# Optimization experiments

Hardware: AMD Instinct MI355X
Metric: run time of the kernel (lower is better)

The kernel has to match this reference:

```python
import jax, jax.numpy as jnp
import numpy as np

B, FEAT, FIELD, K = 16384, 2048, 32, 64

def setup_inputs() -> dict:
    key = jax.random.key(0)
    k1, k2, k3, k4 = jax.random.split(key, 4)
    x = jax.random.normal(k1, (B, FEAT), dtype=jnp.float32)
    # nn.Linear(feature_size, 1): weight [1, FEAT] (use vector), bias [1] (scalar)
    w = jax.random.normal(k2, (FEAT,), dtype=jnp.float32) / np.sqrt(FEAT)
    b = jax.random.normal(k3, (), dtype=jnp.float32)
    # v ~ N(0, 0.01) as in torch.normal(0, 0.01, ...)
    v = 0.01 * jax.random.normal(k4, (FEAT, FIELD, K), dtype=jnp.float32)
    return {"x": x, "w": w, "b": b, "v": v}

def reference(x, w, b, v):
    # linear part: Linear(feature_size, 1).squeeze() -> [B]
    linear_part = x @ w + b  # [B]
    # field_x = tensordot(x, v, dims=1) -> [B, FIELD, K]
    field_x = jnp.einsum('bf,fsk->bsk', x, v)
    # sum_{i<j} sum_k f_i * f_j  ==  0.5 * (||sum_i f_i||^2 - sum_i ||f_i||^2)
    s = field_x.sum(axis=1)                      # [B, K]
    sq = (field_x * field_x).sum(axis=(1, 2))    # [B]
    interaction = 0.5 * ((s * s).sum(axis=-1) - sq)  # [B]
    return jax.nn.sigmoid(linear_part + interaction)
```

## Files before the change

### kernel.cpp

```cpp
#include <hip/hip_runtime.h>
#include <cstdint>
#include <cstddef>

#define B_ROWS 16384
#define FEAT   2048
#define FIELD  32
#define KDIM   64
#define NCOLS  2048
#define NAUG   2176

using half8   = __attribute__((ext_vector_type(8))) _Float16;
using half4   = __attribute__((ext_vector_type(4))) _Float16;
using floatx4 = __attribute__((ext_vector_type(4))) float;

__device__ __forceinline__ void load_lds16(const void* g, void* l) {
  __builtin_amdgcn_global_load_lds((const __attribute__((address_space(1))) void*)g,
                                   (__attribute__((address_space(3))) void*)l, 16, 0, 0);
}

__global__ __launch_bounds__(256) void k_prep_v(const float* __restrict__ v,
                                                const float* __restrict__ w,
                                                _Float16* __restrict__ vt,
                                                float* __restrict__ arg) {
  const int bb = blockIdx.x;
  const int t = threadIdx.x;
  if (bb < 1024) {
    __shared__ _Float16 tile[64 * 68];
    const int f0 = (bb >> 5) * 64;
    const int n0 = (bb & 31) * 64;
#pragma unroll
    for (int j = 0; j < 4; ++j) {
      int c = j * 256 + t;
      int row = c >> 4;
      int col = (c & 15) * 4;
      float4 val = *(const float4*)(v + (size_t)(f0 + row) * NCOLS + n0 + col);
      tile[row * 68 + col + 0] = (_Float16)val.x;
      tile[row * 68 + col + 1] = (_Float16)val.y;
      tile[row * 68 + col + 2] = (_Float16)val.z;
      tile[row * 68 + col + 3] = (_Float16)val.w;
    }
    __syncthreads();
#pragma unroll
    for (int j = 0; j < 4; ++j) {
      int c = j * 256 + t;
      int nl = c >> 4;
      int fl = (c & 15) * 4;
      half4 h = { tile[(fl + 0) * 68 + nl], tile[(fl + 1) * 68 + nl],
                  tile[(fl + 2) * 68 + nl], tile[(fl + 3) * 68 + nl] };
      *(half4*)(vt + (size_t)(n0 + nl) * FEAT + f0 + fl) = h;
    }
  } else if (bb < 1536) {
    const int k = t & 63;
    const int f = (bb - 1024) * 4 + (t >> 6);
    float s = 0.f;
#pragma unroll
    for (int si = 0; si < FIELD; ++si) s += v[(size_t)f * NCOLS + si * KDIM + k];
    vt[(size_t)(NCOLS + k) * FEAT + f] = (_Float16)s;
  } else if (bb < 2048) {
    int idx = (bb - 1536) * 256 + t;
    int r = NCOLS + KDIM + (idx >> 11);
    int f = idx & 2047;
    vt[(size_t)r * FEAT + f] = (r == NCOLS + KDIM) ? (_Float16)w[f] : (_Float16)0.f;
  } else {
    arg[(bb - 2048) * 256 + t] = 0.f;
  }
}

__global__ __launch_bounds__(256) void k_prep_xa(const float* __restrict__ x,
                                                 const _Float16* __restrict__ vt,
                                                 _Float16* __restrict__ xh,
                                                 float* __restrict__ arg) {
  __shared__ __align__(16) _Float16 lds_a[32 * 64];
  __shared__ __align__(16) _Float16 lds_b[128 * 64];
  const int t = threadIdx.x;
  const int m0 = blockIdx.x * 32;
  const int lane = t & 63;
  const int wave = t >> 6;
  const int wm = (wave & 1) * 16;
  const int wn = (wave >> 1) * 64;
  const int lr = lane & 15;
  const int lk = (lane >> 4) * 8;

  const int arow = t >> 3;
  const int akc  = t & 7;
  const float*    xsrc = x  + (size_t)(m0 + arow) * FEAT + akc * 8;
  _Float16*       xdst = xh + (size_t)(m0 + arow) * FEAT + akc * 8;
  _Float16*       adst = lds_a + arow * 64 + (akc ^ (arow & 7)) * 8;

  floatx4 acc[4] = {};

  for (int k0 = 0; k0 < FEAT; k0 += 64) {
    float4 va = *(const float4*)(xsrc + k0);
    float4 vb = *(const float4*)(xsrc + k0 + 4);
    half8 h = { (_Float16)va.x, (_Float16)va.y, (_Float16)va.z, (_Float16)va.w,
                (_Float16)vb.x, (_Float16)vb.y, (_Float16)vb.z, (_Float16)vb.w };
    *(half8*)(xdst + k0) = h;
    *(half8*)adst = h;
#pragma unroll
    for (int i = 0; i < 4; ++i) {
      int c = i * 256 + t;
      int row = c >> 3;
      int g = (c & 7) ^ (row & 7);
      load_lds16(vt + (size_t)(NCOLS + row) * FEAT + k0 + g * 8, lds_b + c * 8);
    }
    __syncthreads();
#pragma unroll
    for (int ks = 0; ks < 64; ks += 32) {
      const int kc = (ks + lk) >> 3;
      const int ma = wm + lr;
      half8 af = *(const half8*)(lds_a + ma * 64 + (kc ^ (ma & 7)) * 8);
      half8 bf[4];
#pragma unroll
      for (int f = 0; f < 4; ++f) {
        int nb = wn + f * 16 + lr;
        bf[f] = *(const half8*)(lds_b + nb * 64 + (kc ^ (nb & 7)) * 8);
      }
#pragma unroll
      for (int fn = 0; fn < 4; ++fn)
        acc[fn] = __builtin_amdgcn_mfma_f32_16x16x32_f16(af, bf[fn],
                                                         acc[fn], 0, 0, 0);
    }
    __syncthreads();
  }

  const int cq = lane >> 4;
#pragma unroll
  for (int r = 0; r < 4; ++r) {
    float contrib = 0.f;
#pragma unroll
    for (int fn = 0; fn < 4; ++fn) {
      int col = wn + fn * 16 + lr;
      float vv = acc[fn][r];
      if (col < KDIM)            contrib += 0.5f * vv * vv;
      else if (col == KDIM)      contrib += vv;
    }
    contrib += __shfl_xor(contrib, 1);
    contrib += __shfl_xor(contrib, 2);
    contrib += __shfl_xor(contrib, 4);
    contrib += __shfl_xor(contrib, 8);
    if (lr == 0) atomicAdd(&arg[m0 + wm + cq * 4 + r], contrib);
  }
}

__global__ __launch_bounds__(512, 2) void k_gemm(const _Float16* __restrict__ xh,
                                                 const _Float16* __restrict__ vt,
                                                 float* __restrict__ arg) {
  __shared__ __align__(16) _Float16 lds[65536];
  const int tid  = threadIdx.x;
  const int lane = tid & 63;
  const int wave = tid >> 6;
  const int wm   = wave >> 2;
  const int wn   = wave & 3;
  const int lr   = lane & 15;
  const int q    = lane >> 4;

  const int bid = blockIdx.x;
  const int wg  = (bid & 7) * 64 + (bid >> 3);
  const int ng  = wg >> 7;
  const int rem = wg & 127;
  const int mi  = rem >> 1;
  const int nr  = rem & 1;
  const int m0  = mi * 256;
  const int n0  = (ng * 2 + nr) * 256;

  int offA[4], offB[4];
#pragma unroll
  for (int f = 0; f < 4; ++f) {
    int L = f * 16 + lr;
    int u = wm * 4 + q;
    offA[f] = L * 64 + ((u ^ (L & 7)) * 8);
  }
#pragma unroll
  for (int g = 0; g < 4; ++g) {
    int L = (wn & 1) * 64 + g * 16 + lr;
    int u = (wn >> 1) * 4 + q;
    offB[g] = L * 64 + ((u ^ (L & 7)) * 8);
  }

  const int L0   = tid >> 3;
  const int u0   = (tid & 7) ^ (L0 & 7);
  const int row0 = (u0 >> 2) * 128 + L0;
  const int kc0  = u0 & 3;
  const _Float16* pA0 = xh + (size_t)(m0 + row0) * FEAT + kc0 * 8;
  const _Float16* pA1 = pA0 + (size_t)64 * FEAT;
  const _Float16* pB0 = vt + (size_t)(n0 + row0) * FEAT + kc0 * 8;
  const _Float16* pB1 = pB0 + (size_t)64 * FEAT;

  auto stageA = [&](int koff, int seg) {
    load_lds16(pA0 + koff, lds + seg + tid * 8);
    load_lds16(pA1 + koff, lds + seg + 4096 + tid * 8);
  };
  auto stageB = [&](int koff, int seg) {
    load_lds16(pB0 + koff, lds + seg + tid * 8);
    load_lds16(pB1 + koff, lds + seg + 4096 + tid * 8);
  };

  floatx4 acc[8][4] = {};
  half8 af[4], bf[4];

  stageA(0, 0);       stageB(0, 32768);
  stageA(32, 8192);   stageB(32, 40960);
  stageA(64, 16384);  stageB(64, 49152);
  asm volatile("s_waitcnt vmcnt(4)" ::: "memory");
  __builtin_amdgcn_s_barrier();

#define PHASE_TAIL()                                        \
    __builtin_amdgcn_s_barrier();                           \
    asm volatile("s_waitcnt lgkmcnt(0)" ::: "memory");      \
    __builtin_amdgcn_sched_barrier(0);                      \
    __builtin_amdgcn_s_setprio(1)

#define PHASE_END()                                         \
    __builtin_amdgcn_s_setprio(0);                          \
    __builtin_amdgcn_s_barrier()

#pragma unroll 2
  for (int t = 0; t < 32; ++t) {
    const int sA0  = ((t & 1) << 1) * 8192;
    const int sB0  = 32768 + sA0;
    const int sPA1 = ((((t + 1) & 1) << 1) | 1) * 8192;

#pragma unroll
    for (int g = 0; g < 4; ++g) bf[g] = *(const half8*)(lds + sB0 + offB[g]);
#pragma unroll
    for (int f = 0; f < 4; ++f) af[f] = *(const half8*)(lds + sA0 + offA[f]);
    if (t < 31) stageA((t + 1) * 64 + 32, sPA1);
    PHASE_TAIL();
#pragma unroll
    for (int f = 0; f < 4; ++f)
#pragma unroll
      for (int g = 0; g < 4; ++g)
        acc[f][g] = __builtin_amdgcn_mfma_f32_16x16x32_f16(af[f], bf[g],
                                                           acc[f][g], 0, 0, 0);
    PHASE_END();

#pragma unroll
    for (int f = 0; f < 4; ++f) af[f] = *(const half8*)(lds + sA0 + 4096 + offA[f]);
    if (t < 31) stageB((t + 1) * 64 + 32, 32768 + sPA1);
    PHASE_TAIL();
#pragma unroll
    for (int f = 0; f < 4; ++f)
#pragma unroll
      for (int g = 0; g < 4; ++g)
        acc[4 + f][g] = __builtin_amdgcn_mfma_f32_16x16x32_f16(af[f], bf[g],
                                                               acc[4 + f][g], 0, 0, 0);
    PHASE_END();

#pragma unroll
    for (int g = 0; g < 4; ++g) bf[g] = *(const half8*)(lds + sB0 + 8192 + offB[g]);
#pragma unroll
    for (int f = 0; f < 4; ++f) af[f] = *(const half8*)(lds + sA0 + 8192 + offA[f]);
    if (t < 30) stageA((t + 2) * 64, sA0);
    PHASE_TAIL();
#pragma unroll
    for (int f = 0; f < 4; ++f)
#pragma unroll
      for (int g = 0; g < 4; ++g)
        acc[f][g] = __builtin_amdgcn_mfma_f32_16x16x32_f16(af[f], bf[g],
                                                           acc[f][g], 0, 0, 0);
    PHASE_END();

#pragma unroll
    for (int f = 0; f < 4; ++f) af[f] = *(const half8*)(lds + sA0 + 12288 + offA[f]);
    if (t < 30) stageB((t + 2) * 64, sB0);
    __builtin_amdgcn_s_barrier();
    asm volatile("s_waitcnt lgkmcnt(0)" ::: "memory");
    __builtin_amdgcn_sched_barrier(0);
    __builtin_amdgcn_s_setprio(1);
#pragma unroll
    for (int f = 0; f < 4; ++f)
#pragma unroll
      for (int g = 0; g < 4; ++g)
        acc[4 + f][g] = __builtin_amdgcn_mfma_f32_16x16x32_f16(af[f], bf[g],
                                                               acc[4 + f][g], 0, 0, 0);
    __builtin_amdgcn_s_setprio(0);
    if (t < 30) { asm volatile("s_waitcnt vmcnt(4)" ::: "memory"); }
    else        { asm volatile("s_waitcnt vmcnt(0)" ::: "memory"); }
    __builtin_amdgcn_sched_barrier(0);
    __builtin_amdgcn_s_barrier();
  }
#undef PHASE_TAIL
#undef PHASE_END

  const int cq = lane >> 4;
  const int mrow = m0 + wm * 128;
#pragma unroll
  for (int f = 0; f < 8; ++f) {
#pragma unroll
    for (int r = 0; r < 4; ++r) {
      float contrib = 0.f;
#pragma unroll
      for (int g = 0; g < 4; ++g) {
        float vv = acc[f][g][r];
        contrib -= 0.5f * vv * vv;
      }
      contrib += __shfl_xor(contrib, 1);
      contrib += __shfl_xor(contrib, 2);
      contrib += __shfl_xor(contrib, 4);
      contrib += __shfl_xor(contrib, 8);
      if (lr == 0) atomicAdd(&arg[mrow + f * 16 + cq * 4 + r], contrib);
    }
  }
}

__global__ __launch_bounds__(256) void k_fin(const float* __restrict__ arg,
                                             const float* __restrict__ b,
                                             float* __restrict__ out) {
  int i = blockIdx.x * 256 + threadIdx.x;
  float z = arg[i] + b[0];
  out[i] = 1.f / (1.f + __expf(-z));
}

extern "C" void kernel_launch(void* const* d_in, const int* in_sizes, int n_in,
                              void* d_out, int out_size, void* d_ws, size_t ws_size,
                              hipStream_t stream) {
  const float* x = (const float*)d_in[0];
  const float* w = (const float*)d_in[1];
  const float* b = (const float*)d_in[2];
  const float* v = (const float*)d_in[3];
  float* out = (float*)d_out;

  char* ws = (char*)d_ws;
  _Float16* xh  = (_Float16*)ws;
  _Float16* vt  = (_Float16*)(ws + 67108864);
  float*    arg = (float*)(ws + 67108864 + 8912896);

  k_prep_v<<<2112, 256, 0, stream>>>(v, w, vt, arg);
  k_prep_xa<<<512, 256, 0, stream>>>(x, vt, xh, arg);
  k_gemm<<<512, 512, 0, stream>>>(xh, vt, arg);
  k_fin<<<64, 256, 0, stream>>>(arg, b, out);
}
```

Measured before the change: 354.9 us.

## Double-buffer MFMA fragments so LDS reads overlap the previous MFMA phase

```diff
diff --git a/kernel.cpp b/kernel.cpp
--- a/kernel.cpp
+++ b/kernel.cpp
@@ -142,6 +142,14 @@
   }
 }
 
+#define NT 32
+
+#define VMCNT(N) asm volatile("s_waitcnt vmcnt(" #N ")" ::: "memory")
+#define LGKM0()  asm volatile("s_waitcnt lgkmcnt(0)" ::: "memory")
+#define SCHED0() __builtin_amdgcn_sched_barrier(0)
+#define BARRIER() __builtin_amdgcn_s_barrier()
+#define PRIO(N) __builtin_amdgcn_s_setprio(N)
+
 __global__ __launch_bounds__(512, 2) void k_gemm(const _Float16* __restrict__ xh,
                                                  const _Float16* __restrict__ vt,
                                                  float* __restrict__ arg) {
@@ -196,91 +204,93 @@
   };
 
   floatx4 acc[8][4] = {};
-  half8 af[4], bf[4];
+  half8 afP[4], afQ[4], bf0[4], bf1[4];
 
   stageA(0, 0);       stageB(0, 32768);
   stageA(32, 8192);   stageB(32, 40960);
   stageA(64, 16384);  stageB(64, 49152);
-  asm volatile("s_waitcnt vmcnt(4)" ::: "memory");
-  __builtin_amdgcn_s_barrier();
-
-#define PHASE_TAIL()                                        \
-    __builtin_amdgcn_s_barrier();                           \
-    asm volatile("s_waitcnt lgkmcnt(0)" ::: "memory");      \
-    __builtin_amdgcn_sched_barrier(0);                      \
-    __builtin_amdgcn_s_setprio(1)
-
-#define PHASE_END()                                         \
-    __builtin_amdgcn_s_setprio(0);                          \
-    __builtin_amdgcn_s_barrier()
+  VMCNT(8);
+  BARRIER();
+  SCHED0();
+#pragma unroll
+  for (int f = 0; f < 4; ++f) afP[f] = *(const half8*)(lds + offA[f]);
+#pragma unroll
+  for (int g = 0; g < 4; ++g) bf0[g] = *(const half8*)(lds + 32768 + offB[g]);
 
 #pragma unroll 2
-  for (int t = 0; t < 32; ++t) {
-    const int sA0  = ((t & 1) << 1) * 8192;
+  for (int t = 0; t < NT; ++t) {
+    const int sA0  = (t & 1) << 14;
+    const int sA1  = sA0 + 8192;
     const int sB0  = 32768 + sA0;
-    const int sPA1 = ((((t + 1) & 1) << 1) | 1) * 8192;
-
-#pragma unroll
-    for (int g = 0; g < 4; ++g) bf[g] = *(const half8*)(lds + sB0 + offB[g]);
-#pragma unroll
-    for (int f = 0; f < 4; ++f) af[f] = *(const half8*)(lds + sA0 + offA[f]);
-    if (t < 31) stageA((t + 1) * 64 + 32, sPA1);
-    PHASE_TAIL();
+    const int sB1  = sB0 + 8192;
+    const int nsA0 = sA0 ^ 16384;
+    const int nsA1 = nsA0 + 8192;
+    const int nsB0 = 32768 + nsA0;
+    const int nsB1 = nsB0 + 8192;
+
+    BARRIER(); SCHED0();
+#pragma unroll
+    for (int f = 0; f < 4; ++f) afQ[f] = *(const half8*)(lds + sA0 + 4096 + offA[f]);
+    if (t + 1 < NT) stageA((t + 1) * 64 + 32, nsA1);
+    SCHED0(); PRIO(1);
 #pragma unroll
     for (int f = 0; f < 4; ++f)
 #pragma unroll
       for (int g = 0; g < 4; ++g)
-        acc[f][g] = __builtin_amdgcn_mfma_f32_16x16x32_f16(af[f], bf[g],
+        acc[f][g] = __builtin_amdgcn_mfma_f32_16x16x32_f16(afP[f], bf0[g],
                                                            acc[f][g], 0, 0, 0);
-    PHASE_END();
-
-#pragma unroll
-    for (int f = 0; f < 4; ++f) af[f] = *(const half8*)(lds + sA0 + 4096 + offA[f]);
-    if (t < 31) stageB((t + 1) * 64 + 32, 32768 + sPA1);
-    PHASE_TAIL();
+    PRIO(0); SCHED0();
+    LGKM0();
+    if (t < NT - 1) { VMCNT(6); } else { VMCNT(0); }
+
+    BARRIER(); SCHED0();
+#pragma unroll
+    for (int f = 0; f < 4; ++f) afP[f] = *(const half8*)(lds + sA1 + offA[f]);
+#pragma unroll
+    for (int g = 0; g < 4; ++g) bf1[g] = *(const half8*)(lds + sB1 + offB[g]);
+    if (t + 1 < NT) stageB((t + 1) * 64 + 32, nsB1);
+    SCHED0(); PRIO(1);
 #pragma unroll
     for (int f = 0; f < 4; ++f)
 #pragma unroll
       for (int g = 0; g < 4; ++g)
-        acc[4 + f][g] = __builtin_amdgcn_mfma_f32_16x16x32_f16(af[f], bf[g],
+        acc[4 + f][g] = __builtin_amdgcn_mfma_f32_16x16x32_f16(afQ[f], bf0[g],
                                                                acc[4 + f][g], 0, 0, 0);
-    PHASE_END();
-
-#pragma unroll
-    for (int g = 0; g < 4; ++g) bf[g] = *(const half8*)(lds + sB0 + 8192 + offB[g]);
-#pragma unroll
-    for (int f = 0; f < 4; ++f) af[f] = *(const half8*)(lds + sA0 + 8192 + offA[f]);
-    if (t < 30) stageA((t + 2) * 64, sA0);
-    PHASE_TAIL();
+    PRIO(0); SCHED0();
+
+    BARRIER(); SCHED0();
+#pragma unroll
+    for (int f = 0; f < 4; ++f) afQ[f] = *(const half8*)(lds + sA1 + 4096 + offA[f]);
+    if (t + 2 < NT) stageA((t + 2) * 64, sA0);
+    SCHED0(); PRIO(1);
 #pragma unroll
     for (int f = 0; f < 4; ++f)
 #pragma unroll
       for (int g = 0; g < 4; ++g)
-        acc[f][g] = __builtin_amdgcn_mfma_f32_16x16x32_f16(af[f], bf[g],
+        acc[f][g] = __builtin_amdgcn_mfma_f32_16x16x32_f16(afP[f], bf1[g],
                                                            acc[f][g], 0, 0, 0);
-    PHASE_END();
-
-#pragma unroll
-    for (int f = 0; f < 4; ++f) af[f] = *(const half8*)(lds + sA0 + 12288 + offA[f]);
-    if (t < 30) stageB((t + 2) * 64, sB0);
-    __builtin_amdgcn_s_barrier();
-    asm volatile("s_waitcnt lgkmcnt(0)" ::: "memory");
-    __builtin_amdgcn_sched_barrier(0);
-    __builtin_amdgcn_s_setprio(1);
+    PRIO(0); SCHED0();
+    LGKM0();
+    if (t < NT - 2)       { VMCNT(6); }
+    else if (t == NT - 2) { VMCNT(4); }
+
+    BARRIER(); SCHED0();
+    if (t + 1 < NT) {
+#pragma unroll
+      for (int f = 0; f < 4; ++f) afP[f] = *(const half8*)(lds + nsA0 + offA[f]);
+#pragma unroll
+      for (int g = 0; g < 4; ++g) bf0[g] = *(const half8*)(lds + nsB0 + offB[g]);
+    }
+    if (t + 2 < NT) stageB((t + 2) * 64, sB0);
+    SCHED0(); PRIO(1);
 #pragma unroll
     for (int f = 0; f < 4; ++f)
 #pragma unroll
       for (int g = 0; g < 4; ++g)
-        acc[4 + f][g] = __builtin_amdgcn_mfma_f32_16x16x32_f16(af[f], bf[g],
+        acc[4 + f][g] = __builtin_amdgcn_mfma_f32_16x16x32_f16(afQ[f], bf1[g],
                                                                acc[4 + f][g], 0, 0, 0);
-    __builtin_amdgcn_s_setprio(0);
-    if (t < 30) { asm volatile("s_waitcnt vmcnt(4)" ::: "memory"); }
-    else        { asm volatile("s_waitcnt vmcnt(0)" ::: "memory"); }
-    __builtin_amdgcn_sched_barrier(0);
-    __builtin_amdgcn_s_barrier();
-  }
-#undef PHASE_TAIL
-#undef PHASE_END
+    PRIO(0); SCHED0();
+  }
 
   const int cq = lane >> 4;
   const int mrow = m0 + wm * 128;
```

Measured after the change: 518.6 us. +46.1%, slower.
